# Optimization experiments

Measured on AMD Instinct MI355X. Metric: run time of the kernel, lower is better.

Reference implementation:

```python
import jax, jax.numpy as jnp
import numpy as np

EPS = 1e-5

def prelu(x, a):
    return jnp.where(x >= 0, x, a * x)

def batch_norm(x, axes):
    # training-mode BatchNorm with gamma=1, beta=0 (init values)
    m = jnp.mean(x, axis=axes, keepdims=True)
    v = jnp.var(x, axis=axes, keepdims=True)
    return (x - m) / jnp.sqrt(v + EPS)

def conv_branch(X, w, b):
    # X: [B,N,F]; Conv2d(1,1,(1,k)) over the feature axis, VALID
    lhs = X[:, None, :, :]                      # [B,1,N,F]
    rhs = w.reshape(1, 1, 1, -1)                # OIHW
    out = jax.lax.conv_general_dilated(lhs, rhs, (1, 1), 'VALID',
        dimension_numbers=('NCHW', 'OIHW', 'NCHW'))
    return out[:, 0] + b                        # [B,N,F-k+1]

def setup_inputs() -> dict:
    key = jax.random.key(0)
    ks = jax.random.split(key, 16)
    B, N, F, H, D = 8192, 29, 147, 4, 128
    d_cat = 429
    s = 0.05
    return {
        'X': jax.random.normal(ks[0], (B, N, F), jnp.float32),
        'corr': jax.random.uniform(ks[1], (B, N, N), jnp.float32),
        'w_c1': s * jax.random.normal(ks[2], (3,), jnp.float32),
        'b_c1': jnp.zeros((1,), jnp.float32),
        'w_c2': s * jax.random.normal(ks[3], (5,), jnp.float32),
        'b_c2': jnp.zeros((1,), jnp.float32),
        'w_c3': s * jax.random.normal(ks[4], (7,), jnp.float32),
        'b_c3': jnp.zeros((1,), jnp.float32),
        'a_cnn': 0.25 * jnp.ones((1,), jnp.float32),
        'Wg': s * jax.random.normal(ks[5], (d_cat, D), jnp.float32),
        'bg': jnp.zeros((D,), jnp.float32),
        'a_gnn': 0.25 * jnp.ones((1,), jnp.float32),
        'centroids': jax.random.normal(ks[6], (H, 1, D), jnp.float32),
        'head_w': s * jax.random.normal(ks[7], (H,), jnp.float32),
        'Wp': s * jax.random.normal(ks[8], (D, D), jnp.float32),
        'bp': jnp.zeros((D,), jnp.float32),
        'Wm1': s * jax.random.normal(ks[9], (D, D), jnp.float32),
        'bm1': jnp.zeros((D,), jnp.float32),
        'a_mlp': 0.25 * jnp.ones((1,), jnp.float32),
        'Wm2': s * jax.random.normal(ks[10], (D, 1), jnp.float32),
        'bm2': jnp.zeros((1,), jnp.float32),
    }

def reference(X, corr, w_c1, b_c1, w_c2, b_c2, w_c3, b_c3, a_cnn,
              Wg, bg, a_gnn, centroids, head_w, Wp, bp,
              Wm1, bm1, a_mlp, Wm2, bm2):
    # three conv branches + concat + PReLU + BN over node channels
    a1 = conv_branch(X, w_c1, b_c1)             # [B,29,145]
    a2 = conv_branch(X, w_c2, b_c2)             # [B,29,143]
    a3 = conv_branch(X, w_c3, b_c3)             # [B,29,141]
    x = prelu(jnp.concatenate([a1, a2, a3], axis=2), a_cnn)  # [B,29,429]
    x = batch_norm(x, (0, 2))
    # GraphConv: A x W + b
    x = jnp.einsum('bnm,bmd->bnd', corr, x) @ Wg + bg        # [B,29,128]
    x = prelu(x, a_gnn)
    x = batch_norm(x, (0, 2))
    # CoSimPool: multi-head cosine-sim attention assignment to 1 cluster
    xn = x / (jnp.linalg.norm(x, axis=-1, keepdims=True) + 1e-8)
    cn = centroids / (jnp.linalg.norm(centroids, axis=-1, keepdims=True) + 1e-8)
    sim = jnp.einsum('hmd,bnd->bhmn', cn, xn)                # [B,4,1,29]
    agg = jnp.einsum('h,bhmn->bmn', head_w, sim)             # 1x1 conv over heads
    C = jax.nn.softmax(agg, axis=-1)                         # [B,1,29]
    x = jnp.einsum('bmn,bnd->bmd', C, x) @ Wp + bp           # [B,1,128]
    x = x[:, 0]                                              # squeeze(1)
    x = batch_norm(x, (0,))
    h = prelu(x @ Wm1 + bm1, a_mlp)
    y = jax.nn.sigmoid(h @ Wm2 + bm2)                        # [B,1]
    return y
```

## Files before the change

### kernel.cpp

```cpp
#include <hip/hip_runtime.h>

#define B_    8192
#define N_    29
#define F_    147
#define DC    429
#define D_    128
#define ROWS  (B_*N_)
#define EPSBN 1e-5f

#define UTSTR   4096
#define RS_SH   3712

#define X3_OFF   16777216
#define ACC_OFF  (X3_OFF + B_*D_)
#define BN1_OFF  (ACC_OFF)
#define BN2_OFF  (ACC_OFF + 1856)
#define BN3_OFF  (ACC_OFF + 3712)
#define FIN_OFF  (ACC_OFF + 11904)
#define CSW_OFF  (FIN_OFF + 384)
#define V_OFF    (FIN_OFF + 512)
#define V1_OFF   (FIN_OFF + 640)
#define CSWP_OFF (FIN_OFF + 768)
#define IMG_OFF  (FIN_OFF + 1024)
#define WPI_OFF  (IMG_OFF + 28672)
#define WM1I_OFF (WPI_OFF + 8192)

typedef __bf16 bf16x8 __attribute__((ext_vector_type(8)));
typedef float  f32x4  __attribute__((ext_vector_type(4)));

__device__ __forceinline__ unsigned short f2bf(float f) {
  __bf16 h = (__bf16)f;
  return __builtin_bit_cast(unsigned short, h);
}
__device__ __forceinline__ float bf2f(unsigned u16) {
  return __uint_as_float(u16 << 16);
}

#define TSTR 456
#define UTILS 34
#define ATSTR 136

__global__ void k0a_img(const float* __restrict__ Wg, const float* __restrict__ Wp,
                        const float* __restrict__ Wm1, float* __restrict__ ws)
{
  const int tid = threadIdx.x;
  if (blockIdx.x < 16) {
    __shared__ float cs_l[8];
    const int kb = blockIdx.x * 8;
    if (tid < 8) cs_l[tid] = 0.f;
    __syncthreads();
    unsigned short* img = (unsigned short*)(ws + IMG_OFF);
    for (int i = tid; i < 8*448; i += 256) {
      int kk = i / 448, dk = i - kk*448;
      int k = kb + kk;
      int d;
      if      (dk < 145)  d = dk;
      else if (dk == 145) d = -1;
      else if (dk < 289)  d = dk - 1;
      else if (dk == 289) d = -1;
      else if (dk < 431)  d = dk - 2;
      else                d = -1;
      float v = (d >= 0) ? Wg[(size_t)d*D_ + k] : 0.f;
      img[(size_t)k*448 + dk] = f2bf(v);
      if (d >= 0) atomicAdd(&cs_l[kk], v);
    }
    __syncthreads();
    if (tid < 8) ws[CSW_OFF + kb + tid] = cs_l[tid];
  } else if (blockIdx.x == 16) {
    unsigned short* wpi = (unsigned short*)(ws + WPI_OFF);
    for (int i = tid; i < 16384; i += 256) {
      int k = i >> 7, c = i & 127;
      wpi[c*128 + k] = f2bf(Wp[k*128 + c]);
    }
    if (tid < 128) {
      float s = 0.f;
      for (int k = 0; k < 128; ++k) s += Wp[k*128 + tid];
      ws[CSWP_OFF + tid] = s;
    }
  } else {
    unsigned short* wmi = (unsigned short*)(ws + WM1I_OFF);
    for (int i = tid; i < 16384; i += 256) {
      int k = i >> 7, c = i & 127;
      wmi[c*128 + k] = f2bf(Wm1[k*128 + c]);
    }
  }
}

__global__ void k0b_cent(const float* __restrict__ cent, const float* __restrict__ hw,
                         float* __restrict__ ws)
{
  __shared__ float sq[128];
  __shared__ float nrm;
  const int tid = threadIdx.x;
  float vk = 0.f;
  for (int h = 0; h < 4; ++h) {
    float c = cent[h*D_ + tid];
    sq[tid] = c*c;
    __syncthreads();
    if (tid == 0) { float s=0.f; for (int j=0;j<128;++j) s+=sq[j]; nrm = sqrtf(s)+1e-8f; }
    __syncthreads();
    vk += hw[h] * c / nrm;
    __syncthreads();
  }
  ws[V_OFF + tid] = vk;
  sq[tid] = vk;
  __syncthreads();
  if (tid == 0) { float s=0.f; for (int j=0;j<128;++j) s+=sq[j]; ws[V1_OFF] = s; }
}

__global__ __launch_bounds__(256, 5) void k1_conv_gemm(
    const float* __restrict__ X,
    const float* __restrict__ wc1, const float* __restrict__ bc1,
    const float* __restrict__ wc2, const float* __restrict__ bc2,
    const float* __restrict__ wc3, const float* __restrict__ bc3,
    const float* __restrict__ acnn, float* __restrict__ ws)
{
  __shared__ __align__(16) unsigned short t_s[32*TSTR];
  const int tid = threadIdx.x;
  const int b = blockIdx.x;

  {
    float* xs = (float*)t_s;
    const float* Xb = X + (size_t)b * (N_ * F_);
    for (int i = tid; i < 29*147; i += 256) {
      int rr = i / 147;
      int cc = i - rr*147;
      xs[rr*148 + cc] = Xb[i];
    }
  }
  __syncthreads();

  const float c10 = wc1[0], c11 = wc1[1], c12 = wc1[2], b1 = bc1[0];
  const float c20 = wc2[0], c21 = wc2[1], c22 = wc2[2], c23 = wc2[3], c24 = wc2[4], b2 = bc2[0];
  const float c30 = wc3[0], c31 = wc3[1], c32 = wc3[2], c33 = wc3[3], c34 = wc3[4],
              c35 = wc3[5], c36 = wc3[6], b3 = bc3[0];
  const float ap = acnn[0];

  const int nC = tid >> 3, qC = tid & 7;
  const bool act = (nC < 29);
  const int f0 = qC * 19;
  const int nld = act ? nC : 28;
  float xv[25];
  {
    const float* xrow = (const float*)t_s + nld*148 + f0;
    #pragma unroll
    for (int i = 0; i < 25; ++i) xv[i] = xrow[i];
  }
  __syncthreads();

  for (int i = tid; i < 3*448; i += 256) {
    int r = i / 448, c = i - r*448;
    t_s[(29 + r)*TSTR + c] = 0;
  }
  for (int i = tid; i < 29*19; i += 256) {
    int n = i / 19, j = i - n*19;
    int col = (j == 0) ? 145 : ((j == 1) ? 289 : (429 + j));
    t_s[n*TSTR + col] = 0;
  }

  {
    float s1 = 0.f, s2 = 0.f;
    unsigned short* tr = t_s + nC*TSTR;
    if (act) {
      if (qC < 7) {
        #pragma unroll
        for (int i = 0; i < 19; ++i) {
          float v1 = fmaf(xv[i],c10, fmaf(xv[i+1],c11, fmaf(xv[i+2],c12, b1)));
          v1 = (v1 >= 0.f) ? v1 : ap*v1;
          s1 += v1; s2 = fmaf(v1, v1, s2);
          tr[f0 + i] = f2bf(v1);
          float v2 = fmaf(xv[i],c20, fmaf(xv[i+1],c21, fmaf(xv[i+2],c22, fmaf(xv[i+3],c23, fmaf(xv[i+4],c24, b2)))));
          v2 = (v2 >= 0.f) ? v2 : ap*v2;
          s1 += v2; s2 = fmaf(v2, v2, s2);
          tr[146 + f0 + i] = f2bf(v2);
          float v3 = fmaf(xv[i],c30, fmaf(xv[i+1],c31, fmaf(xv[i+2],c32, fmaf(xv[i+3],c33, fmaf(xv[i+4],c34, fmaf(xv[i+5],c35, fmaf(xv[i+6],c36, b3)))))));
          v3 = (v3 >= 0.f) ? v3 : ap*v3;
          s1 += v3; s2 = fmaf(v3, v3, s2);
          tr[290 + f0 + i] = f2bf(v3);
        }
      } else {
        #pragma unroll
        for (int i = 0; i < 12; ++i) {
          float v1 = fmaf(xv[i],c10, fmaf(xv[i+1],c11, fmaf(xv[i+2],c12, b1)));
          v1 = (v1 >= 0.f) ? v1 : ap*v1;
          s1 += v1; s2 = fmaf(v1, v1, s2);
          tr[133 + i] = f2bf(v1);
        }
        #pragma unroll
        for (int i = 0; i < 10; ++i) {
          float v2 = fmaf(xv[i],c20, fmaf(xv[i+1],c21, fmaf(xv[i+2],c22, fmaf(xv[i+3],c23, fmaf(xv[i+4],c24, b2)))));
          v2 = (v2 >= 0.f) ? v2 : ap*v2;
          s1 += v2; s2 = fmaf(v2, v2, s2);
          tr[279 + i] = f2bf(v2);
        }
        #pragma unroll
        for (int i = 0; i < 8; ++i) {
          float v3 = fmaf(xv[i],c30, fmaf(xv[i+1],c31, fmaf(xv[i+2],c32, fmaf(xv[i+3],c33, fmaf(xv[i+4],c34, fmaf(xv[i+5],c35, fmaf(xv[i+6],c36, b3)))))));
          v3 = (v3 >= 0.f) ? v3 : ap*v3;
          s1 += v3; s2 = fmaf(v3, v3, s2);
          tr[423 + i] = f2bf(v3);
        }
      }
    }
    #pragma unroll
    for (int off = 4; off >= 1; off >>= 1) {
      s1 += __shfl_xor(s1, off);
      s2 += __shfl_xor(s2, off);
    }
    if (act && qC == 0) {
      float* bn1 = ws + BN1_OFF + (size_t)(blockIdx.x & 31) * 58;
      atomicAdd(&bn1[nC*2+0], s1);
      atomicAdd(&bn1[nC*2+1], s2);
    }
  }
  __syncthreads();

  const int wv = tid >> 6, lane = tid & 63;
  const int lrow = lane & 15, quad = lane >> 4;
  const int n0 = wv * 32;
  const unsigned short* imgp = (const unsigned short*)(ws + IMG_OFF);
  const unsigned short* gB0 = imgp + (size_t)(n0 + lrow)*448 + quad*8;
  const unsigned short* gB1 = gB0 + 16*448;
  const unsigned short* tA = t_s + quad*8;

  f32x4 a00 = (f32x4){0.f,0.f,0.f,0.f}, a01 = a00, a10 = a00, a11 = a00;
  bf16x8 Br0[2], Br1[2];
  Br0[0] = *(const bf16x8*)(gB0);
  Br1[0] = *(const bf16x8*)(gB1);
  Br0[1] = *(const bf16x8*)(gB0 + 32);
  Br1[1] = *(const bf16x8*)(gB1 + 32);
  #pragma unroll
  for (int ks = 0; ks < 14; ++ks) {
    bf16x8 Bc0 = Br0[ks & 1], Bc1 = Br1[ks & 1];
    if (ks < 12) {
      Br0[ks & 1] = *(const bf16x8*)(gB0 + (ks+2)*32);
      Br1[ks & 1] = *(const bf16x8*)(gB1 + (ks+2)*32);
    }
    bf16x8 A0 = *(const bf16x8*)(tA + lrow*TSTR + ks*32);
    bf16x8 A1 = *(const bf16x8*)(tA + (16+lrow)*TSTR + ks*32);
    a00 = __builtin_amdgcn_mfma_f32_16x16x32_bf16(A0, Bc0, a00, 0, 0, 0);
    a01 = __builtin_amdgcn_mfma_f32_16x16x32_bf16(A0, Bc1, a01, 0, 0, 0);
    a10 = __builtin_amdgcn_mfma_f32_16x16x32_bf16(A1, Bc0, a10, 0, 0, 0);
    a11 = __builtin_amdgcn_mfma_f32_16x16x32_bf16(A1, Bc1, a11, 0, 0, 0);
  }
  __syncthreads();

  {
    unsigned short* ut = t_s;
    const int fb0 = n0 + lrow, fb1 = n0 + 16 + lrow;
    #pragma unroll
    for (int i = 0; i < 4; ++i) {
      int m0 = quad*4 + i, m1 = 16 + quad*4 + i;
      ut[fb0*UTILS + m0] = f2bf(a00[i]);
      ut[fb1*UTILS + m0] = f2bf(a01[i]);
      ut[fb0*UTILS + m1] = f2bf(a10[i]);
      ut[fb1*UTILS + m1] = f2bf(a11[i]);
    }
  }
  __syncthreads();
  {
    const unsigned* u32t = (const unsigned*)t_s;
    unsigned short* ws16 = (unsigned short*)ws;
    unsigned* Ug = (unsigned*)(ws16 + (size_t)b * UTSTR);
    #pragma unroll
    for (int it = 0; it < 8; ++it) {
      int idx = tid + it*256;
      int f = idx >> 4, pr = idx & 15;
      Ug[f*16 + pr] = u32t[f*17 + pr];
    }
  }
}

__global__ void k2_bn1f(float* __restrict__ ws)
{
  const int n = threadIdx.x;
  if (n < 29) {
    float s1 = 0.f, s2 = 0.f;
    #pragma unroll 4
    for (int s = 0; s < 32; ++s) {
      s1 += ws[BN1_OFF + s*58 + n*2 + 0];
      s2 += ws[BN1_OFF + s*58 + n*2 + 1];
    }
    const float inv = 1.f / (float)(B_ * DC);
    float mean = s1 * inv;
    float var  = s2 * inv - mean * mean;
    ws[FIN_OFF + n]      = mean;
    ws[FIN_OFF + 32 + n] = rsqrtf(var + EPSBN);
  }
}

__global__ __launch_bounds__(256) void k3_gnn(
    const float* __restrict__ corr, const float* __restrict__ bg,
    const float* __restrict__ agnn, float* __restrict__ ws)
{
  __shared__ float cwf[841];
  __shared__ unsigned short a_s[32*40];
  __shared__ float m1s[29], is1s[29], cms[32], st1s[29], st2s[29], svs[29];

  const int b = blockIdx.x, tid = threadIdx.x;
  const int wv = tid >> 6, lane = tid & 63;
  const int lrow = lane & 15, quad = lane >> 4;
  unsigned short* Utb = (unsigned short*)ws + (size_t)b * UTSTR;

  const int f0 = wv * 32;
  bf16x8 B0 = *(const bf16x8*)&Utb[(f0      + lrow)*32 + quad*8];
  bf16x8 B1 = *(const bf16x8*)&Utb[(f0 + 16 + lrow)*32 + quad*8];

  if (tid < 29) {
    m1s[tid]  = ws[FIN_OFF + tid];
    is1s[tid] = ws[FIN_OFF + 32 + tid];
    st1s[tid] = 0.f; st2s[tid] = 0.f; svs[tid] = 0.f;
  }
  const float* cb = corr + (size_t)b * 841;
  for (int i = tid; i < 841; i += 256) cwf[i] = cb[i];
  __syncthreads();

  #pragma unroll
  for (int it = 0; it < 4; ++it) {
    int i = tid + it*256;
    int n = i >> 5, m = i & 31;
    bool val = (n < 29 && m < 29);
    float v = val ? cwf[n*29 + m] * is1s[m] : 0.f;
    a_s[n*40 + m] = f2bf(v);
    float p = val ? v * m1s[m] : 0.f;
    #pragma unroll
    for (int off = 16; off >= 1; off >>= 1) p += __shfl_xor(p, off);
    if (m == 0 && n < 29) cms[n] = p;
  }
  __syncthreads();

  bf16x8 A0 = *(const bf16x8*)&a_s[lrow*40 + quad*8];
  bf16x8 A1 = *(const bf16x8*)&a_s[(16 + lrow)*40 + quad*8];
  f32x4 acc[2][2];
  acc[0][0] = (f32x4){0.f,0.f,0.f,0.f}; acc[0][1] = (f32x4){0.f,0.f,0.f,0.f};
  acc[1][0] = (f32x4){0.f,0.f,0.f,0.f}; acc[1][1] = (f32x4){0.f,0.f,0.f,0.f};
  acc[0][0] = __builtin_amdgcn_mfma_f32_16x16x32_bf16(A0, B0, acc[0][0], 0, 0, 0);
  acc[0][1] = __builtin_amdgcn_mfma_f32_16x16x32_bf16(A0, B1, acc[0][1], 0, 0, 0);
  acc[1][0] = __builtin_amdgcn_mfma_f32_16x16x32_bf16(A1, B0, acc[1][0], 0, 0, 0);
  acc[1][1] = __builtin_amdgcn_mfma_f32_16x16x32_bf16(A1, B1, acc[1][1], 0, 0, 0);
  __syncthreads();

  const float ag = agnn[0];
  const float vA  = ws[V_OFF  + f0 + lrow],      vB  = ws[V_OFF  + f0 + 16 + lrow];
  const float csA = ws[CSW_OFF + f0 + lrow],     csB = ws[CSW_OFF + f0 + 16 + lrow];
  const float bgA = bg[f0 + lrow],               bgB = bg[f0 + 16 + lrow];
  #pragma unroll
  for (int mt = 0; mt < 2; ++mt) {
    #pragma unroll
    for (int i = 0; i < 4; ++i) {
      int n = mt*16 + quad*4 + i;
      if (n < 29) {
        float y0 = acc[mt][0][i] - cms[n]*csA + bgA;
        float y1 = acc[mt][1][i] - cms[n]*csB + bgB;
        y0 = (y0 >= 0.f) ? y0 : ag*y0;
        y1 = (y1 >= 0.f) ? y1 : ag*y1;
        Utb[n*D_ + f0 + lrow]      = f2bf(y0);
        Utb[n*D_ + f0 + 16 + lrow] = f2bf(y1);
        float sy  = y0 + y1;
        float sy2 = fmaf(y0, y0, y1*y1);
        float sv  = fmaf(y0, vA, y1*vB);
        #pragma unroll
        for (int off = 8; off >= 1; off >>= 1) {
          sy  += __shfl_xor(sy, off);
          sy2 += __shfl_xor(sy2, off);
          sv  += __shfl_xor(sv, off);
        }
        if (lrow == 0) {
          atomicAdd(&st1s[n], sy);
          atomicAdd(&st2s[n], sy2);
          atomicAdd(&svs[n],  sv);
        }
      }
    }
  }
  __syncthreads();
  if (tid < 29) {
    float* rs = (float*)(Utb + RS_SH);
    rs[tid]      = st1s[tid];
    rs[29 + tid] = st2s[tid];
    rs[58 + tid] = svs[tid];
    float* bn2 = ws + BN2_OFF + (size_t)(b & 31) * 58;
    atomicAdd(&bn2[tid*2+0], st1s[tid]);
    atomicAdd(&bn2[tid*2+1], st2s[tid]);
  }
}

__global__ __launch_bounds__(256) void k4_pool(
    const float* __restrict__ bpv, float* __restrict__ ws)
{
  __shared__ unsigned short Atile[32*ATSTR];
  __shared__ float m2s[29], is2s[29], koffs[32];
  const int tid = threadIdx.x, wv = tid >> 6, lane = tid & 63;
  const int b0 = blockIdx.x * 32;
  const unsigned short* U16 = (const unsigned short*)ws;

  if (tid < 29) {
    float s1 = 0.f, s2 = 0.f;
    #pragma unroll 4
    for (int s = 0; s < 32; ++s) {
      s1 += ws[BN2_OFF + s*58 + tid*2 + 0];
      s2 += ws[BN2_OFF + s*58 + tid*2 + 1];
    }
    const float inv = 1.f / (float)(B_ * D_);
    float mean = s1 * inv, var = s2 * inv - mean * mean;
    m2s[tid] = mean; is2s[tid] = rsqrtf(var + EPSBN);
  }
  __syncthreads();

  const float V1 = ws[V1_OFF];
  unsigned* At32 = (unsigned*)Atile;
  for (int mb = 0; mb < 8; ++mb) {
    const int m = wv*8 + mb;
    const unsigned short* yb = U16 + (size_t)(b0 + m) * UTSTR;
    const float* rs = (const float*)(yb + RS_SH);
    float agg = -1e30f, m2 = 0.f, is2 = 0.f;
    if (lane < 29) {
      float S1 = rs[lane], S2 = rs[29+lane], Sv = rs[58+lane];
      m2 = m2s[lane]; is2 = is2s[lane];
      float ss = fmaxf(S2 - 2.f*m2*S1 + 128.f*m2*m2, 0.f);
      agg = (is2*(Sv - m2*V1)) / (is2*sqrtf(ss) + 1e-8f);
    }
    float mx = agg;
    #pragma unroll
    for (int off = 32; off >= 1; off >>= 1) mx = fmaxf(mx, __shfl_xor(mx, off));
    float e = (lane < 29) ? __expf(agg - mx) : 0.f;
    float den = e, kof = e*is2*m2;
    #pragma unroll
    for (int off = 32; off >= 1; off >>= 1) { den += __shfl_xor(den, off); kof += __shfl_xor(kof, off); }
    float rden = 1.f / den;
    float c = e * is2 * rden;
    if (lane == 0) koffs[m] = kof * rden;
    const unsigned* y32 = (const unsigned*)yb;
    float p0 = 0.f, p1 = 0.f;
    #pragma unroll
    for (int n = 0; n < 29; ++n) {
      float cn = __shfl(c, n);
      unsigned u = y32[n*64 + lane];
      p0 = fmaf(cn, bf2f(u & 0xffffu), p0);
      p1 = fmaf(cn, bf2f(u >> 16), p1);
    }
    At32[m*68 + lane] = (unsigned)f2bf(p0) | ((unsigned)f2bf(p1) << 16);
  }
  __syncthreads();

  const int lrow = lane & 15, quad = lane >> 4;
  const int n0 = wv * 32;
  const unsigned short* wpi = (const unsigned short*)(ws + WPI_OFF);
  f32x4 acc[2][2];
  acc[0][0] = (f32x4){0.f,0.f,0.f,0.f}; acc[0][1] = acc[0][0];
  acc[1][0] = acc[0][0]; acc[1][1] = acc[0][0];
  #pragma unroll
  for (int ks = 0; ks < 4; ++ks) {
    bf16x8 A0 = *(const bf16x8*)&Atile[lrow*ATSTR + ks*32 + quad*8];
    bf16x8 A1 = *(const bf16x8*)&Atile[(16+lrow)*ATSTR + ks*32 + quad*8];
    bf16x8 Bq0 = *(const bf16x8*)&wpi[(size_t)(n0 + lrow)*128 + ks*32 + quad*8];
    bf16x8 Bq1 = *(const bf16x8*)&wpi[(size_t)(n0 + 16 + lrow)*128 + ks*32 + quad*8];
    acc[0][0] = __builtin_amdgcn_mfma_f32_16x16x32_bf16(A0, Bq0, acc[0][0], 0, 0, 0);
    acc[0][1] = __builtin_amdgcn_mfma_f32_16x16x32_bf16(A0, Bq1, acc[0][1], 0, 0, 0);
    acc[1][0] = __builtin_amdgcn_mfma_f32_16x16x32_bf16(A1, Bq0, acc[1][0], 0, 0, 0);
    acc[1][1] = __builtin_amdgcn_mfma_f32_16x16x32_bf16(A1, Bq1, acc[1][1], 0, 0, 0);
  }

  float* bn3 = ws + BN3_OFF + (size_t)(blockIdx.x & 31) * 256;
  #pragma unroll
  for (int nt = 0; nt < 2; ++nt) {
    int col = n0 + nt*16 + lrow;
    float cswp = ws[CSWP_OFF + col], bp = bpv[col];
    float s1c = 0.f, s2c = 0.f;
    #pragma unroll
    for (int mt = 0; mt < 2; ++mt) {
      #pragma unroll
      for (int i = 0; i < 4; ++i) {
        int m = mt*16 + quad*4 + i;
        float x3 = acc[mt][nt][i] - koffs[m]*cswp + bp;
        ws[X3_OFF + (size_t)(b0 + m)*D_ + col] = x3;
        s1c += x3; s2c = fmaf(x3, x3, s2c);
      }
    }
    s1c += __shfl_xor(s1c, 16); s1c += __shfl_xor(s1c, 32);
    s2c += __shfl_xor(s2c, 16); s2c += __shfl_xor(s2c, 32);
    if (quad == 0) {
      atomicAdd(&bn3[col*2+0], s1c);
      atomicAdd(&bn3[col*2+1], s2c);
    }
  }
}

__global__ __launch_bounds__(256) void k5_mlp(
    const float* __restrict__ bm1, const float* __restrict__ amlp,
    const float* __restrict__ Wm2, const float* __restrict__ bm2,
    float* __restrict__ ws, float* __restrict__ out)
{
  __shared__ unsigned short Atile[32*ATSTR];
  __shared__ float m3s[128], is3s[128], logit_s[32];
  const int tid = threadIdx.x, wv = tid >> 6, lane = tid & 63;
  const int b0 = blockIdx.x * 32;

  if (tid < 128) {
    float s1 = 0.f, s2 = 0.f;
    #pragma unroll 4
    for (int s = 0; s < 32; ++s) {
      s1 += ws[BN3_OFF + s*256 + tid*2 + 0];
      s2 += ws[BN3_OFF + s*256 + tid*2 + 1];
    }
    const float inv = 1.f / (float)B_;
    float mean = s1 * inv, var = s2 * inv - mean * mean;
    m3s[tid] = mean; is3s[tid] = rsqrtf(var + EPSBN);
  }
  if (tid >= 128 && tid < 160) logit_s[tid-128] = 0.f;
  __syncthreads();

  for (int it = 0; it < 16; ++it) {
    int idx = tid + it*256;
    int row = idx >> 7, col = idx & 127;
    float v = (ws[X3_OFF + (size_t)(b0+row)*D_ + col] - m3s[col]) * is3s[col];
    Atile[row*ATSTR + col] = f2bf(v);
  }
  __syncthreads();

  const int lrow = lane & 15, quad = lane >> 4;
  const int n0 = wv * 32;
  const unsigned short* wmi = (const unsigned short*)(ws + WM1I_OFF);
  f32x4 acc[2][2];
  acc[0][0] = (f32x4){0.f,0.f,0.f,0.f}; acc[0][1] = acc[0][0];
  acc[1][0] = acc[0][0]; acc[1][1] = acc[0][0];
  #pragma unroll
  for (int ks = 0; ks < 4; ++ks) {
    bf16x8 A0 = *(const bf16x8*)&Atile[lrow*ATSTR + ks*32 + quad*8];
    bf16x8 A1 = *(const bf16x8*)&Atile[(16+lrow)*ATSTR + ks*32 + quad*8];
    bf16x8 Bq0 = *(const bf16x8*)&wmi[(size_t)(n0 + lrow)*128 + ks*32 + quad*8];
    bf16x8 Bq1 = *(const bf16x8*)&wmi[(size_t)(n0 + 16 + lrow)*128 + ks*32 + quad*8];
    acc[0][0] = __builtin_amdgcn_mfma_f32_16x16x32_bf16(A0, Bq0, acc[0][0], 0, 0, 0);
    acc[0][1] = __builtin_amdgcn_mfma_f32_16x16x32_bf16(A0, Bq1, acc[0][1], 0, 0, 0);
    acc[1][0] = __builtin_amdgcn_mfma_f32_16x16x32_bf16(A1, Bq0, acc[1][0], 0, 0, 0);
    acc[1][1] = __builtin_amdgcn_mfma_f32_16x16x32_bf16(A1, Bq1, acc[1][1], 0, 0, 0);
  }

  const float am = amlp[0];
  float bmc[2], wm2c[2];
  #pragma unroll
  for (int nt = 0; nt < 2; ++nt) {
    int col = n0 + nt*16 + lrow;
    bmc[nt] = bm1[col]; wm2c[nt] = Wm2[col];
  }
  #pragma unroll
  for (int mt = 0; mt < 2; ++mt) {
    #pragma unroll
    for (int i = 0; i < 4; ++i) {
      float pm = 0.f;
      #pragma unroll
      for (int nt = 0; nt < 2; ++nt) {
        float h = acc[mt][nt][i] + bmc[nt];
        h = (h >= 0.f) ? h : am*h;
        pm = fmaf(h, wm2c[nt], pm);
      }
      #pragma unroll
      for (int off = 8; off >= 1; off >>= 1) pm += __shfl_xor(pm, off);
      if (lrow == 0) atomicAdd(&logit_s[mt*16 + quad*4 + i], pm);
    }
  }
  __syncthreads();
  if (tid < 32) {
    float logit = logit_s[tid] + bm2[0];
    out[b0 + tid] = 1.f / (1.f + expf(-logit));
  }
}

extern "C" void kernel_launch(void* const* d_in, const int* in_sizes, int n_in,
                              void* d_out, int out_size, void* d_ws, size_t ws_size,
                              hipStream_t stream)
{
  (void)in_sizes; (void)n_in; (void)out_size; (void)ws_size;
  const float* X    = (const float*)d_in[0];
  const float* corr = (const float*)d_in[1];
  const float* wc1  = (const float*)d_in[2];
  const float* bc1  = (const float*)d_in[3];
  const float* wc2  = (const float*)d_in[4];
  const float* bc2  = (const float*)d_in[5];
  const float* wc3  = (const float*)d_in[6];
  const float* bc3  = (const float*)d_in[7];
  const float* acnn = (const float*)d_in[8];
  const float* Wg   = (const float*)d_in[9];
  const float* bg   = (const float*)d_in[10];
  const float* agnn = (const float*)d_in[11];
  const float* cent = (const float*)d_in[12];
  const float* hw   = (const float*)d_in[13];
  const float* Wp   = (const float*)d_in[14];
  const float* bp   = (const float*)d_in[15];
  const float* Wm1  = (const float*)d_in[16];
  const float* bm1  = (const float*)d_in[17];
  const float* amlp = (const float*)d_in[18];
  const float* Wm2  = (const float*)d_in[19];
  const float* bm2  = (const float*)d_in[20];
  float* ws  = (float*)d_ws;
  float* out = (float*)d_out;

  hipMemsetAsync(ws + ACC_OFF, 0, 11904 * sizeof(float), stream);
  k0a_img<<<18, 256, 0, stream>>>(Wg, Wp, Wm1, ws);
  k0b_cent<<<1, 128, 0, stream>>>(cent, hw, ws);
  k1_conv_gemm<<<B_, 256, 0, stream>>>(X, wc1, bc1, wc2, bc2, wc3, bc3, acnn, ws);
  k2_bn1f<<<1, 64, 0, stream>>>(ws);
  k3_gnn<<<B_, 256, 0, stream>>>(corr, bg, agnn, ws);
  k4_pool<<<B_/32, 256, 0, stream>>>(bp, ws);
  k5_mlp<<<B_/32, 256, 0, stream>>>(bm1, amlp, Wm2, bm2, ws, out);
}
```

Baseline: 465.2 us.

## Merge setup kernels, load X via global_load_lds, pack conv math into float2

Folds the memset and centroid-prep kernel into a single setup launch, with extra waves zeroing the accumulators and a wave-shuffle norm reduction. The conv kernel now stages X straight into LDS with global_load_lds (unpadded row stride 147) instead of a per-element loop with divides. It also splits the conv work as 18 columns per thread using packed float2 FMAs and paired bf16 stores, and packs the MFMA output transpose into 32-bit LDS writes. The aim is to cut launch overhead, address arithmetic and VALU/LDS instruction count in the conv stage. In exchange the tail-column handling becomes more intricate and the 4-byte async LDS loads clamp at the end of the buffer.

```diff
diff --git a/kernel.cpp b/kernel.cpp
--- a/kernel.cpp
+++ b/kernel.cpp
@@ -27,6 +27,7 @@
 
 typedef __bf16 bf16x8 __attribute__((ext_vector_type(8)));
 typedef float  f32x4  __attribute__((ext_vector_type(4)));
+typedef float  f32x2  __attribute__((ext_vector_type(2)));
 
 __device__ __forceinline__ unsigned short f2bf(float f) {
   __bf16 h = (__bf16)f;
@@ -35,13 +36,29 @@
 __device__ __forceinline__ float bf2f(unsigned u16) {
   return __uint_as_float(u16 << 16);
 }
+__device__ __forceinline__ unsigned packbf(f32x2 v) {
+  return (unsigned)f2bf(v[0]) | ((unsigned)f2bf(v[1]) << 16);
+}
+__device__ __forceinline__ f32x2 pfma(f32x2 a, float s, f32x2 c) {
+  return __builtin_elementwise_fma(a, (f32x2){s, s}, c);
+}
+__device__ __forceinline__ f32x2 prelu2(f32x2 v, float a) {
+  f32x2 z = (f32x2){0.f, 0.f};
+  return __builtin_elementwise_fma(__builtin_elementwise_min(v, z), (f32x2){a, a},
+                                   __builtin_elementwise_max(v, z));
+}
+__device__ __forceinline__ void gload_lds4(const float* g, void* l) {
+  __builtin_amdgcn_global_load_lds((const __attribute__((address_space(1))) void*)g,
+                                   (__attribute__((address_space(3))) void*)l, 4, 0, 0);
+}
 
 #define TSTR 456
 #define UTILS 34
 #define ATSTR 136
 
-__global__ void k0a_img(const float* __restrict__ Wg, const float* __restrict__ Wp,
-                        const float* __restrict__ Wm1, float* __restrict__ ws)
+__global__ void k0_setup(const float* __restrict__ Wg, const float* __restrict__ Wp,
+                         const float* __restrict__ Wm1, const float* __restrict__ cent,
+                         const float* __restrict__ hw, float* __restrict__ ws)
 {
   const int tid = threadIdx.x;
   if (blockIdx.x < 16) {
@@ -77,35 +94,36 @@
       for (int k = 0; k < 128; ++k) s += Wp[k*128 + tid];
       ws[CSWP_OFF + tid] = s;
     }
-  } else {
+  } else if (blockIdx.x == 17) {
     unsigned short* wmi = (unsigned short*)(ws + WM1I_OFF);
     for (int i = tid; i < 16384; i += 256) {
       int k = i >> 7, c = i & 127;
       wmi[c*128 + k] = f2bf(Wm1[k*128 + c]);
     }
-  }
-}
-
-__global__ void k0b_cent(const float* __restrict__ cent, const float* __restrict__ hw,
-                         float* __restrict__ ws)
-{
-  __shared__ float sq[128];
-  __shared__ float nrm;
-  const int tid = threadIdx.x;
-  float vk = 0.f;
-  for (int h = 0; h < 4; ++h) {
-    float c = cent[h*D_ + tid];
-    sq[tid] = c*c;
-    __syncthreads();
-    if (tid == 0) { float s=0.f; for (int j=0;j<128;++j) s+=sq[j]; nrm = sqrtf(s)+1e-8f; }
-    __syncthreads();
-    vk += hw[h] * c / nrm;
-    __syncthreads();
-  }
-  ws[V_OFF + tid] = vk;
-  sq[tid] = vk;
-  __syncthreads();
-  if (tid == 0) { float s=0.f; for (int j=0;j<128;++j) s+=sq[j]; ws[V1_OFF] = s; }
+  } else {
+    const int wv = tid >> 6, lane = tid & 63;
+    if (wv == 0) {
+      float vk0 = 0.f, vk1 = 0.f;
+      for (int h = 0; h < 4; ++h) {
+        float c0 = cent[h*D_ + lane];
+        float c1 = cent[h*D_ + 64 + lane];
+        float s = c0*c0 + c1*c1;
+        #pragma unroll
+        for (int off = 32; off >= 1; off >>= 1) s += __shfl_xor(s, off);
+        float w = hw[h] / (sqrtf(s) + 1e-8f);
+        vk0 = fmaf(c0, w, vk0);
+        vk1 = fmaf(c1, w, vk1);
+      }
+      ws[V_OFF + lane]      = vk0;
+      ws[V_OFF + 64 + lane] = vk1;
+      float t = vk0 + vk1;
+      #pragma unroll
+      for (int off = 32; off >= 1; off >>= 1) t += __shfl_xor(t, off);
+      if (lane == 0) ws[V1_OFF] = t;
+    } else {
+      for (int i = tid - 64; i < 11904; i += 192) ws[ACC_OFF + i] = 0.f;
+    }
+  }
 }
 
 __global__ __launch_bounds__(256, 5) void k1_conv_gemm(
@@ -118,14 +136,20 @@
   __shared__ __align__(16) unsigned short t_s[32*TSTR];
   const int tid = threadIdx.x;
   const int b = blockIdx.x;
+  const int wv = tid >> 6, lane = tid & 63;
+  const int lrow = lane & 15, quad = lane >> 4;
 
   {
-    float* xs = (float*)t_s;
     const float* Xb = X + (size_t)b * (N_ * F_);
-    for (int i = tid; i < 29*147; i += 256) {
-      int rr = i / 147;
-      int cc = i - rr*147;
-      xs[rr*148 + cc] = Xb[i];
+    unsigned* xd = (unsigned*)t_s;
+    #pragma unroll
+    for (int t = 0; t < 17; ++t) {
+      int c = wv + 4*t;
+      if (c < 67) {
+        int dw = c*64 + lane;
+        int src = (dw < 4263) ? dw : 4262;
+        gload_lds4(Xb + src, xd + (size_t)c*64);
+      }
     }
   }
   __syncthreads();
@@ -138,13 +162,13 @@
 
   const int nC = tid >> 3, qC = tid & 7;
   const bool act = (nC < 29);
-  const int f0 = qC * 19;
+  const int f0 = qC * 18;
   const int nld = act ? nC : 28;
-  float xv[25];
+  float xv[24];
   {
-    const float* xrow = (const float*)t_s + nld*148 + f0;
-    #pragma unroll
-    for (int i = 0; i < 25; ++i) xv[i] = xrow[i];
+    const float* xrow = (const float*)t_s + nld*147 + f0;
+    #pragma unroll
+    for (int i = 0; i < 24; ++i) xv[i] = xrow[i];
   }
   __syncthreads();
 
@@ -159,49 +183,61 @@
   }
 
   {
-    float s1 = 0.f, s2 = 0.f;
-    unsigned short* tr = t_s + nC*TSTR;
+    f32x2 s1v = (f32x2){0.f,0.f}, s2v = (f32x2){0.f,0.f};
+    float s1t = 0.f, s2t = 0.f;
+    unsigned short* tr = t_s + nC*TSTR + f0;
     if (act) {
-      if (qC < 7) {
-        #pragma unroll
-        for (int i = 0; i < 19; ++i) {
-          float v1 = fmaf(xv[i],c10, fmaf(xv[i+1],c11, fmaf(xv[i+2],c12, b1)));
-          v1 = (v1 >= 0.f) ? v1 : ap*v1;
-          s1 += v1; s2 = fmaf(v1, v1, s2);
-          tr[f0 + i] = f2bf(v1);
-          float v2 = fmaf(xv[i],c20, fmaf(xv[i+1],c21, fmaf(xv[i+2],c22, fmaf(xv[i+3],c23, fmaf(xv[i+4],c24, b2)))));
-          v2 = (v2 >= 0.f) ? v2 : ap*v2;
-          s1 += v2; s2 = fmaf(v2, v2, s2);
-          tr[146 + f0 + i] = f2bf(v2);
-          float v3 = fmaf(xv[i],c30, fmaf(xv[i+1],c31, fmaf(xv[i+2],c32, fmaf(xv[i+3],c33, fmaf(xv[i+4],c34, fmaf(xv[i+5],c35, fmaf(xv[i+6],c36, b3)))))));
-          v3 = (v3 >= 0.f) ? v3 : ap*v3;
-          s1 += v3; s2 = fmaf(v3, v3, s2);
-          tr[290 + f0 + i] = f2bf(v3);
+      const int np1 = (qC < 7) ? 9 : 9;
+      const int np2 = (qC < 7) ? 9 : 8;
+      const int np3 = (qC < 7) ? 9 : 7;
+      #pragma unroll
+      for (int j = 0; j < 9; ++j) {
+        const int k = 2*j;
+        f32x2 xA = (f32x2){xv[k],   xv[k+1]};
+        f32x2 xB = (f32x2){xv[k+1], xv[k+2]};
+        f32x2 xC = (f32x2){xv[k+2], xv[k+3]};
+        if (j < np1) {
+          f32x2 v1 = pfma(xA,c10, pfma(xB,c11, pfma(xC,c12, (f32x2){b1,b1})));
+          v1 = prelu2(v1, ap);
+          s1v += v1; s2v = __builtin_elementwise_fma(v1, v1, s2v);
+          *(unsigned*)(tr + k) = packbf(v1);
         }
-      } else {
-        #pragma unroll
-        for (int i = 0; i < 12; ++i) {
-          float v1 = fmaf(xv[i],c10, fmaf(xv[i+1],c11, fmaf(xv[i+2],c12, b1)));
-          v1 = (v1 >= 0.f) ? v1 : ap*v1;
-          s1 += v1; s2 = fmaf(v1, v1, s2);
-          tr[133 + i] = f2bf(v1);
+        if (j < np2) {
+          f32x2 xD = (f32x2){xv[k+3], xv[k+4]};
+          f32x2 xE = (f32x2){xv[k+4], xv[k+5]};
+          f32x2 v2 = pfma(xA,c20, pfma(xB,c21, pfma(xC,c22, pfma(xD,c23, pfma(xE,c24, (f32x2){b2,b2})))));
+          v2 = prelu2(v2, ap);
+          s1v += v2; s2v = __builtin_elementwise_fma(v2, v2, s2v);
+          *(unsigned*)(tr + 146 + k) = packbf(v2);
         }
-        #pragma unroll
-        for (int i = 0; i < 10; ++i) {
-          float v2 = fmaf(xv[i],c20, fmaf(xv[i+1],c21, fmaf(xv[i+2],c22, fmaf(xv[i+3],c23, fmaf(xv[i+4],c24, b2)))));
-          v2 = (v2 >= 0.f) ? v2 : ap*v2;
-          s1 += v2; s2 = fmaf(v2, v2, s2);
-          tr[279 + i] = f2bf(v2);
-        }
-        #pragma unroll
-        for (int i = 0; i < 8; ++i) {
-          float v3 = fmaf(xv[i],c30, fmaf(xv[i+1],c31, fmaf(xv[i+2],c32, fmaf(xv[i+3],c33, fmaf(xv[i+4],c34, fmaf(xv[i+5],c35, fmaf(xv[i+6],c36, b3)))))));
-          v3 = (v3 >= 0.f) ? v3 : ap*v3;
-          s1 += v3; s2 = fmaf(v3, v3, s2);
-          tr[423 + i] = f2bf(v3);
+        if (j < np3) {
+          f32x2 xD = (f32x2){xv[k+3], xv[k+4]};
+          f32x2 xE = (f32x2){xv[k+4], xv[k+5]};
+          f32x2 xF = (f32x2){xv[k+5], xv[k+6]};
+          f32x2 xG = (f32x2){xv[k+6], xv[k+7]};
+          f32x2 v3 = pfma(xA,c30, pfma(xB,c31, pfma(xC,c32, pfma(xD,c33, pfma(xE,c34, pfma(xF,c35, pfma(xG,c36, (f32x2){b3,b3})))))));
+          v3 = prelu2(v3, ap);
+          s1v += v3; s2v = __builtin_elementwise_fma(v3, v3, s2v);
+          *(unsigned*)(tr + 290 + k) = packbf(v3);
         }
       }
-    }
+      if (qC == 7) {
+        float u1 = fmaf(xv[18],c10, fmaf(xv[19],c11, fmaf(xv[20],c12, b1)));
+        u1 = (u1 >= 0.f) ? u1 : ap*u1;
+        s1t += u1; s2t = fmaf(u1, u1, s2t);
+        tr[18] = f2bf(u1);
+        float u2 = fmaf(xv[16],c20, fmaf(xv[17],c21, fmaf(xv[18],c22, fmaf(xv[19],c23, fmaf(xv[20],c24, b2)))));
+        u2 = (u2 >= 0.f) ? u2 : ap*u2;
+        s1t += u2; s2t = fmaf(u2, u2, s2t);
+        tr[146 + 16] = f2bf(u2);
+        float u3 = fmaf(xv[14],c30, fmaf(xv[15],c31, fmaf(xv[16],c32, fmaf(xv[17],c33, fmaf(xv[18],c34, fmaf(xv[19],c35, fmaf(xv[20],c36, b3)))))));
+        u3 = (u3 >= 0.f) ? u3 : ap*u3;
+        s1t += u3; s2t = fmaf(u3, u3, s2t);
+        tr[290 + 14] = f2bf(u3);
+      }
+    }
+    float s1 = s1v[0] + s1v[1] + s1t;
+    float s2 = s2v[0] + s2v[1] + s2t;
     #pragma unroll
     for (int off = 4; off >= 1; off >>= 1) {
       s1 += __shfl_xor(s1, off);
@@ -215,8 +251,6 @@
   }
   __syncthreads();
 
-  const int wv = tid >> 6, lane = tid & 63;
-  const int lrow = lane & 15, quad = lane >> 4;
   const int n0 = wv * 32;
   const unsigned short* imgp = (const unsigned short*)(ws + IMG_OFF);
   const unsigned short* gB0 = imgp + (size_t)(n0 + lrow)*448 + quad*8;
@@ -246,15 +280,15 @@
   __syncthreads();
 
   {
-    unsigned short* ut = t_s;
+    unsigned* ut32 = (unsigned*)t_s;
     const int fb0 = n0 + lrow, fb1 = n0 + 16 + lrow;
     #pragma unroll
-    for (int i = 0; i < 4; ++i) {
-      int m0 = quad*4 + i, m1 = 16 + quad*4 + i;
-      ut[fb0*UTILS + m0] = f2bf(a00[i]);
-      ut[fb1*UTILS + m0] = f2bf(a01[i]);
-      ut[fb0*UTILS + m1] = f2bf(a10[i]);
-      ut[fb1*UTILS + m1] = f2bf(a11[i]);
+    for (int jp = 0; jp < 2; ++jp) {
+      int w = quad*2 + jp;
+      ut32[fb0*17 + w]     = packbf((f32x2){a00[2*jp], a00[2*jp+1]});
+      ut32[fb1*17 + w]     = packbf((f32x2){a01[2*jp], a01[2*jp+1]});
+      ut32[fb0*17 + 8 + w] = packbf((f32x2){a10[2*jp], a10[2*jp+1]});
+      ut32[fb1*17 + 8 + w] = packbf((f32x2){a11[2*jp], a11[2*jp+1]});
     }
   }
   __syncthreads();
@@ -595,9 +629,7 @@
   float* ws  = (float*)d_ws;
   float* out = (float*)d_out;
 
-  hipMemsetAsync(ws + ACC_OFF, 0, 11904 * sizeof(float), stream);
-  k0a_img<<<18, 256, 0, stream>>>(Wg, Wp, Wm1, ws);
-  k0b_cent<<<1, 128, 0, stream>>>(cent, hw, ws);
+  k0_setup<<<19, 256, 0, stream>>>(Wg, Wp, Wm1, cent, hw, ws);
   k1_conv_gemm<<<B_, 256, 0, stream>>>(X, wc1, bc1, wc2, bc2, wc3, bc3, acnn, ws);
   k2_bn1f<<<1, 64, 0, stream>>>(ws);
   k3_gnn<<<B_, 256, 0, stream>>>(corr, bg, agnn, ws);
```

New measurement: 450.8 us. -3.1%, faster.
